# Optimization experiments

Hardware: AMD Instinct MI355X
Metric: run time of the kernel (lower is better)

## Reference

```python
import jax, jax.numpy as jnp
import numpy as np
import math

D_MODEL = 1024
NUM_HEADS = 16
D_K = D_MODEL // NUM_HEADS
SEQ_LEN = 2048
THETA = 10000.0


def _rope_tables(seq_len, d_k, theta):
    # inv_freq over even dims, angles repeated-interleaved to full d_k
    inv_freq = theta ** (-jnp.arange(0, d_k, 2, dtype=jnp.float32) / d_k)  # [d_k/2]
    pos = jnp.arange(seq_len, dtype=jnp.float32)                          # [s]
    angles = pos[:, None] * inv_freq[None, :]                             # [s, d_k/2]
    angles = jnp.repeat(angles, 2, axis=-1)                               # [s, d_k]
    return jnp.cos(angles), jnp.sin(angles)


def _rotate_half(x):
    # interleaved pairs: (x0,x1,x2,x3,...) -> (-x1,x0,-x3,x2,...)
    x_even = x[..., ::2]
    x_odd = x[..., 1::2]
    return jnp.stack([-x_odd, x_even], axis=-1).reshape(x.shape)


def _apply_rope(x, cos, sin):
    # x: [b, h, s, d_k]; cos/sin: [s, d_k]
    return x * cos + _rotate_half(x) * sin


def setup_inputs() -> dict:
    key = jax.random.key(0)
    ks = jax.random.split(key, 5)
    scale = 1.0 / math.sqrt(D_MODEL)
    X = jax.random.normal(ks[0], (2, SEQ_LEN, D_MODEL), dtype=jnp.float32)
    Wq = jax.random.normal(ks[1], (D_MODEL, D_MODEL), dtype=jnp.float32) * scale
    Wk = jax.random.normal(ks[2], (D_MODEL, D_MODEL), dtype=jnp.float32) * scale
    Wv = jax.random.normal(ks[3], (D_MODEL, D_MODEL), dtype=jnp.float32) * scale
    Wo = jax.random.normal(ks[4], (D_MODEL, D_MODEL), dtype=jnp.float32) * scale
    return {"X": X, "Wq": Wq, "Wk": Wk, "Wv": Wv, "Wo": Wo}


def reference(X, Wq, Wk, Wv, Wo):
    b, s, _ = X.shape
    h, dk = NUM_HEADS, D_K

    def proj(W):
        return (X @ W.T).reshape(b, s, h, dk).transpose(0, 2, 1, 3)  # [b,h,s,dk]

    q, k, v = proj(Wq), proj(Wk), proj(Wv)

    cos, sin = _rope_tables(s, dk, THETA)
    q = _apply_rope(q, cos, sin)
    k = _apply_rope(k, cos, sin)

    scores = jnp.einsum('bhid,bhjd->bhij', q, k) / math.sqrt(dk)
    causal = jnp.tril(jnp.ones((s, s), dtype=bool))
    scores = jnp.where(causal[None, None], scores, -jnp.inf)
    probs = jax.nn.softmax(scores, axis=-1)
    attended = jnp.einsum('bhij,bhjd->bhid', probs, v)               # [b,h,s,dk]

    out = attended.transpose(0, 2, 1, 3).reshape(b, s, h * dk)
    return out @ Wo.T
```

## Files before the change

kernel.cpp:

```cpp
#include <hip/hip_runtime.h>
#include <stdint.h>

#define D_MODEL 1024
#define NUM_HEADS 16
#define DK 64
#define SEQ 2048
#define BATCH 2
#define MROWS (BATCH * SEQ)
#define LOG2E 1.4426950408889634f
#define FIXM 14.0f

typedef short bf16x8 __attribute__((ext_vector_type(8)));
typedef float f32x4 __attribute__((ext_vector_type(4)));

__device__ __forceinline__ unsigned short f2bf(float f) {
    unsigned int u = __float_as_uint(f);
    u = (u + 0x7fffu + ((u >> 16) & 1u)) >> 16;
    return (unsigned short)u;
}
__device__ __forceinline__ unsigned short f2bf_trunc(float f) {
    return (unsigned short)(__float_as_uint(f) >> 16);
}
__device__ __forceinline__ float bf2f(unsigned short h) {
    return __uint_as_float(((unsigned int)h) << 16);
}
__device__ __forceinline__ void async16(const void* g, void* l) {
    __builtin_amdgcn_global_load_lds(
        (const __attribute__((address_space(1))) void*)g,
        (__attribute__((address_space(3))) void*)l, 16, 0, 0);
}
#define SWZ64(row, b) ((((row) * 8) + ((b) ^ ((row) & 7))) * 8)

__global__ void cast_all(const float4* __restrict__ X, const float4* __restrict__ Wq,
                         const float4* __restrict__ Wk, const float4* __restrict__ Wv,
                         const float4* __restrict__ Wo, ushort4* __restrict__ Xb,
                         ushort4* __restrict__ Wqkvb, ushort4* __restrict__ Wob) {
    int i = blockIdx.x * blockDim.x + threadIdx.x;
    const float4* src;
    ushort4* dst;
    int off;
    if (i < 1048576) { src = X; dst = Xb; off = i; }
    else if (i < 1310720) { src = Wq; dst = Wqkvb; off = i - 1048576; }
    else if (i < 1572864) { src = Wk; dst = Wqkvb + 262144; off = i - 1310720; }
    else if (i < 1835008) { src = Wv; dst = Wqkvb + 524288; off = i - 1572864; }
    else { src = Wo; dst = Wob; off = i - 1835008; }
    float4 v = src[off];
    ushort4 o;
    o.x = f2bf(v.x); o.y = f2bf(v.y); o.z = f2bf(v.z); o.w = f2bf(v.w);
    dst[off] = o;
}

__global__ __launch_bounds__(256) void gemm_qkv_rope(
    const unsigned short* __restrict__ A, const unsigned short* __restrict__ B,
    unsigned short* __restrict__ Qr, unsigned short* __restrict__ Kr,
    unsigned short* __restrict__ Vt) {
    __shared__ unsigned short As[128 * 64];
    __shared__ unsigned short Bs[128 * 64];
    const int K = D_MODEL, N = 3072;
    const int m0 = blockIdx.y * 128, n0 = blockIdx.x * 128;
    const int t = threadIdx.x;
    const int lane = t & 63, wave = t >> 6;
    const int mA = lane & 15, quad = lane >> 4;
    const int wr = (wave >> 1) * 64, wc = (wave & 1) * 64;

    f32x4 acc[4][4] = {};
    for (int k0 = 0; k0 < K; k0 += 64) {
#pragma unroll
        for (int i = 0; i < 4; ++i) {
            int ch = i * 256 + t;
            int r = ch >> 3, b = (ch & 7) ^ (r & 7);
            async16(A + (size_t)(m0 + r) * K + k0 + b * 8, (char*)As + ch * 16);
            async16(B + (size_t)(n0 + r) * K + k0 + b * 8, (char*)Bs + ch * 16);
        }
        __syncthreads();
#pragma unroll
        for (int kk = 0; kk < 2; ++kk) {
            bf16x8 af[4], bfr[4];
#pragma unroll
            for (int mi = 0; mi < 4; ++mi) {
                int rr = wr + mi * 16 + mA;
                af[mi] = *(const bf16x8*)&As[SWZ64(rr, kk * 4 + quad)];
            }
#pragma unroll
            for (int ni = 0; ni < 4; ++ni) {
                int rr = wc + ni * 16 + mA;
                bfr[ni] = *(const bf16x8*)&Bs[SWZ64(rr, kk * 4 + quad)];
            }
#pragma unroll
            for (int mi = 0; mi < 4; ++mi)
#pragma unroll
                for (int ni = 0; ni < 4; ++ni)
                    acc[mi][ni] = __builtin_amdgcn_mfma_f32_16x16x32_bf16(
                        af[mi], bfr[ni], acc[mi][ni], 0, 0, 0);
        }
        __syncthreads();
    }

    const int sec = n0 >> 10;
    if (sec == 2) {
#pragma unroll
        for (int mi = 0; mi < 4; ++mi)
#pragma unroll
            for (int ni = 0; ni < 4; ++ni) {
                int gm = m0 + wr + mi * 16 + quad * 4;
                int gn = n0 + wc + ni * 16 + mA;
                int d = gn & 1023, h = d >> 6, dk = d & 63;
                int b = gm >> 11, s = gm & 2047;
                ushort4 o;
                o.x = f2bf(acc[mi][ni][0]);
                o.y = f2bf(acc[mi][ni][1]);
                o.z = f2bf(acc[mi][ni][2]);
                o.w = f2bf(acc[mi][ni][3]);
                *(ushort4*)&Vt[((size_t)(b * NUM_HEADS + h) * DK + dk) * SEQ + s] = o;
            }
    } else {
        unsigned short* Dst = (sec == 0) ? Qr : Kr;
#pragma unroll
        for (int ni = 0; ni < 4; ++ni) {
            int gn = n0 + wc + ni * 16 + mA;
            int d = gn & 1023, h = d >> 6, dk = d & 63;
            float invf = __expf(-(float)(dk & ~1) * (9.210340371976184f / 64.0f));
            float sgn = (dk & 1) ? 1.0f : -1.0f;
#pragma unroll
            for (int mi = 0; mi < 4; ++mi) {
#pragma unroll
                for (int r = 0; r < 4; ++r) {
                    int gm = m0 + wr + mi * 16 + quad * 4 + r;
                    int b = gm >> 11, s = gm & 2047;
                    float sn, cs;
                    __sincosf((float)s * invf, &sn, &cs);
                    float val = acc[mi][ni][r];
                    float par = __shfl_xor(val, 1, 64);
                    float outv = val * cs + sgn * par * sn;
                    Dst[((size_t)(b * NUM_HEADS + h) * SEQ + s) * DK + dk] = f2bf(outv);
                }
            }
        }
    }
}

template <int TN, int OUT_BF16>
__global__ __launch_bounds__(256) void gemm_tile(
    const unsigned short* __restrict__ A, const unsigned short* __restrict__ B,
    void* __restrict__ Cout, int M, int N, int K) {
    __shared__ unsigned short As[128 * 64];
    __shared__ unsigned short Bs[TN * 64];
    const int m0 = blockIdx.y * 128, n0 = blockIdx.x * TN;
    const int t = threadIdx.x;
    const int lane = t & 63, wave = t >> 6;
    const int mA = lane & 15, quad = lane >> 4;
    constexpr int MI = (TN == 128) ? 4 : 2;
    constexpr int NI = 4;
    const int wr = (TN == 128) ? (wave >> 1) * 64 : wave * 32;
    const int wc = (TN == 128) ? (wave & 1) * 64 : 0;

    f32x4 acc[MI][NI] = {};
    for (int k0 = 0; k0 < K; k0 += 64) {
#pragma unroll
        for (int i = 0; i < 4; ++i) {
            int ch = i * 256 + t;
            int r = ch >> 3, b = (ch & 7) ^ (r & 7);
            async16(A + (size_t)(m0 + r) * K + k0 + b * 8, (char*)As + ch * 16);
        }
#pragma unroll
        for (int i = 0; i < TN / 32; ++i) {
            int ch = i * 256 + t;
            int r = ch >> 3, b = (ch & 7) ^ (r & 7);
            async16(B + (size_t)(n0 + r) * K + k0 + b * 8, (char*)Bs + ch * 16);
        }
        __syncthreads();
#pragma unroll
        for (int kk = 0; kk < 2; ++kk) {
            bf16x8 af[MI], bfr[NI];
#pragma unroll
            for (int mi = 0; mi < MI; ++mi) {
                int rr = wr + mi * 16 + mA;
                af[mi] = *(const bf16x8*)&As[SWZ64(rr, kk * 4 + quad)];
            }
#pragma unroll
            for (int ni = 0; ni < NI; ++ni) {
                int rr = wc + ni * 16 + mA;
                bfr[ni] = *(const bf16x8*)&Bs[SWZ64(rr, kk * 4 + quad)];
            }
#pragma unroll
            for (int mi = 0; mi < MI; ++mi)
#pragma unroll
                for (int ni = 0; ni < NI; ++ni)
                    acc[mi][ni] = __builtin_amdgcn_mfma_f32_16x16x32_bf16(
                        af[mi], bfr[ni], acc[mi][ni], 0, 0, 0);
        }
        __syncthreads();
    }
#pragma unroll
    for (int mi = 0; mi < MI; ++mi)
#pragma unroll
        for (int ni = 0; ni < NI; ++ni)
#pragma unroll
            for (int r = 0; r < 4; ++r) {
                int gm = m0 + wr + mi * 16 + quad * 4 + r;
                int gn = n0 + wc + ni * 16 + mA;
                if (OUT_BF16)
                    ((unsigned short*)Cout)[(size_t)gm * N + gn] = f2bf(acc[mi][ni][r]);
                else
                    ((float*)Cout)[(size_t)gm * N + gn] = acc[mi][ni][r];
            }
}

__global__ __launch_bounds__(256, 4) void flash_attn6(
    const unsigned short* __restrict__ Qr, const unsigned short* __restrict__ Kr,
    const unsigned short* __restrict__ Vt, unsigned short* __restrict__ Att) {
    __shared__ unsigned short Ks[2][64 * 64];
    __shared__ unsigned short Vs[2][64 * 64];
    __shared__ unsigned short Ps[4][16 * 64];
    const int bh = blockIdx.x;
    const int qt = 31 - (int)blockIdx.y;
    const int t = threadIdx.x;
    const int lane = t & 63, wave = t >> 6;
    const int mA = lane & 15, quad = lane >> 4;
    const int qr0 = qt * 64 + wave * 16;
    const size_t qkbase = (size_t)bh * SEQ * DK;
    const unsigned short* Kg = Kr + qkbase;
    const unsigned short* Vg = Vt + (size_t)bh * DK * SEQ;

    bf16x8 aq[2];
#pragma unroll
    for (int c = 0; c < 2; ++c) {
        bf16x8 raw = *(const bf16x8*)&Qr[qkbase + (size_t)(qr0 + mA) * DK + c * 32 + quad * 8];
        bf16x8 s;
#pragma unroll
        for (int j = 0; j < 8; ++j)
            s[j] = (short)f2bf(bf2f((unsigned short)raw[j]) * (0.125f * LOG2E));
        aq[c] = s;
    }

    f32x4 accT[4] = {};
    float lsum[4] = {};

#pragma unroll
    for (int i = 0; i < 2; ++i) {
        int ch = i * 256 + t;
        int row = ch >> 3, sb = (ch & 7) ^ (row & 7);
        async16(Kg + (size_t)row * DK + sb * 8, (char*)Ks[0] + ch * 16);
        async16(Vg + (size_t)row * SEQ + sb * 8, (char*)Vs[0] + ch * 16);
    }

    for (int jt = 0; jt <= qt; ++jt) {
        __syncthreads();
        const int cur = jt & 1;
        if (jt < qt) {
            const int j1 = (jt + 1) * 64;
#pragma unroll
            for (int i = 0; i < 2; ++i) {
                int ch = i * 256 + t;
                int row = ch >> 3, sb = (ch & 7) ^ (row & 7);
                async16(Kg + (size_t)(j1 + row) * DK + sb * 8, (char*)Ks[cur ^ 1] + ch * 16);
                async16(Vg + (size_t)row * SEQ + j1 + sb * 8, (char*)Vs[cur ^ 1] + ch * 16);
            }
        }
        const int j0 = jt * 64;
        const unsigned short* Kt = Ks[cur];
        const unsigned short* Vtile = Vs[cur];
        unsigned short* Pw = Ps[wave];

        f32x4 sc[4] = {};
#pragma unroll
        for (int js = 0; js < 4; ++js) {
            int row = js * 16 + mA;
            bf16x8 b0 = *(const bf16x8*)&Kt[SWZ64(row, quad)];
            bf16x8 b1 = *(const bf16x8*)&Kt[SWZ64(row, quad + 4)];
            sc[js] = __builtin_amdgcn_mfma_f32_16x16x32_bf16(aq[0], b0, sc[js], 0, 0, 0);
            sc[js] = __builtin_amdgcn_mfma_f32_16x16x32_bf16(aq[1], b1, sc[js], 0, 0, 0);
        }
        if (jt == qt) {
#pragma unroll
            for (int js = 0; js < 4; ++js) {
                int gcol = j0 + js * 16 + mA;
#pragma unroll
                for (int r = 0; r < 4; ++r)
                    if (gcol > qr0 + quad * 4 + r) sc[js][r] = -1e30f;
            }
        }

#pragma unroll
        for (int js = 0; js < 4; ++js)
#pragma unroll
            for (int r = 0; r < 4; ++r) {
                float p = __builtin_amdgcn_exp2f(sc[js][r] - FIXM);
                lsum[r] += p;
                int q = quad * 4 + r;
                Pw[SWZ64(q, js * 2 + (mA >> 3)) + (mA & 7)] = f2bf_trunc(p);
            }
        bf16x8 ap0 = *(const bf16x8*)&Pw[SWZ64(mA, quad)];
        bf16x8 ap1 = *(const bf16x8*)&Pw[SWZ64(mA, quad + 4)];
#pragma unroll
        for (int tn = 0; tn < 4; ++tn) {
            int row = tn * 16 + mA;
            bf16x8 bv0 = *(const bf16x8*)&Vtile[SWZ64(row, quad)];
            bf16x8 bv1 = *(const bf16x8*)&Vtile[SWZ64(row, quad + 4)];
            accT[tn] = __builtin_amdgcn_mfma_f32_16x16x32_bf16(bv0, ap0, accT[tn], 0, 0, 0);
            accT[tn] = __builtin_amdgcn_mfma_f32_16x16x32_bf16(bv1, ap1, accT[tn], 0, 0, 0);
        }
    }

#pragma unroll
    for (int r = 0; r < 4; ++r)
#pragma unroll
        for (int off = 1; off < 16; off <<= 1)
            lsum[r] += __shfl_xor(lsum[r], off, 64);
    __syncthreads();
    float* LL = (float*)Ks;
    if (mA == 0)
#pragma unroll
        for (int r = 0; r < 4; ++r) LL[wave * 16 + quad * 4 + r] = lsum[r];
    __syncthreads();
    const float rl = 1.0f / LL[wave * 16 + mA];

    const int b = bh >> 4, h = bh & 15;
#pragma unroll
    for (int tn = 0; tn < 4; ++tn) {
        ushort4 o;
        o.x = f2bf(accT[tn][0] * rl);
        o.y = f2bf(accT[tn][1] * rl);
        o.z = f2bf(accT[tn][2] * rl);
        o.w = f2bf(accT[tn][3] * rl);
        *(ushort4*)&Att[(size_t)(b * SEQ + qr0 + mA) * D_MODEL + h * DK + tn * 16 + quad * 4] = o;
    }
}

extern "C" void kernel_launch(void* const* d_in, const int* in_sizes, int n_in,
                              void* d_out, int out_size, void* d_ws, size_t ws_size,
                              hipStream_t stream) {
    const float* X = (const float*)d_in[0];
    const float* Wq = (const float*)d_in[1];
    const float* Wk = (const float*)d_in[2];
    const float* Wv = (const float*)d_in[3];
    const float* Wo = (const float*)d_in[4];

    char* ws = (char*)d_ws;
    unsigned short* Xb    = (unsigned short*)(ws + 0);
    unsigned short* Wqkvb = (unsigned short*)(ws + (8u << 20));
    unsigned short* Wob   = (unsigned short*)(ws + (14u << 20));
    unsigned short* Qr    = (unsigned short*)(ws + (16u << 20));
    unsigned short* Kr    = (unsigned short*)(ws + (24u << 20));
    unsigned short* Vt    = (unsigned short*)(ws + (32u << 20));
    unsigned short* Att   = (unsigned short*)(ws + (40u << 20));

    cast_all<<<8192, 256, 0, stream>>>((const float4*)X, (const float4*)Wq,
                                       (const float4*)Wk, (const float4*)Wv,
                                       (const float4*)Wo, (ushort4*)Xb,
                                       (ushort4*)Wqkvb, (ushort4*)Wob);

    gemm_qkv_rope<<<dim3(3072 / 128, MROWS / 128), 256, 0, stream>>>(
        Xb, Wqkvb, Qr, Kr, Vt);

    flash_attn6<<<dim3(BATCH * NUM_HEADS, 32), 256, 0, stream>>>(Qr, Kr, Vt, Att);

    gemm_tile<64, 0><<<dim3(D_MODEL / 64, MROWS / 128), 256, 0, stream>>>(
        Att, Wob, d_out, MROWS, D_MODEL, D_MODEL);
}
```

Measured before the change: 182.6 us.

## Enlarge flash-attention query tile and use precomputed RoPE table in QKV epilogue

```diff
diff --git a/kernel.cpp b/kernel.cpp
--- a/kernel.cpp
+++ b/kernel.cpp
@@ -34,34 +34,51 @@
 __global__ void cast_all(const float4* __restrict__ X, const float4* __restrict__ Wq,
                          const float4* __restrict__ Wk, const float4* __restrict__ Wv,
                          const float4* __restrict__ Wo, ushort4* __restrict__ Xb,
-                         ushort4* __restrict__ Wqkvb, ushort4* __restrict__ Wob) {
-    int i = blockIdx.x * blockDim.x + threadIdx.x;
-    const float4* src;
-    ushort4* dst;
-    int off;
-    if (i < 1048576) { src = X; dst = Xb; off = i; }
-    else if (i < 1310720) { src = Wq; dst = Wqkvb; off = i - 1048576; }
-    else if (i < 1572864) { src = Wk; dst = Wqkvb + 262144; off = i - 1310720; }
-    else if (i < 1835008) { src = Wv; dst = Wqkvb + 524288; off = i - 1572864; }
-    else { src = Wo; dst = Wob; off = i - 1835008; }
-    float4 v = src[off];
-    ushort4 o;
-    o.x = f2bf(v.x); o.y = f2bf(v.y); o.z = f2bf(v.z); o.w = f2bf(v.w);
-    dst[off] = o;
+                         ushort4* __restrict__ Wqkvb, ushort4* __restrict__ Wob,
+                         float2* __restrict__ RT) {
+    const int bx = blockIdx.x, t = threadIdx.x;
+    if (bx < 8192) {
+        int i = bx * 256 + t;
+        const float4* src;
+        ushort4* dst;
+        int off;
+        if (i < 1048576) { src = X; dst = Xb; off = i; }
+        else if (i < 1310720) { src = Wq; dst = Wqkvb; off = i - 1048576; }
+        else if (i < 1572864) { src = Wk; dst = Wqkvb + 262144; off = i - 1310720; }
+        else if (i < 1835008) { src = Wv; dst = Wqkvb + 524288; off = i - 1572864; }
+        else { src = Wo; dst = Wob; off = i - 1835008; }
+        float4 v = src[off];
+        ushort4 o;
+        o.x = f2bf(v.x); o.y = f2bf(v.y); o.z = f2bf(v.z); o.w = f2bf(v.w);
+        dst[off] = o;
+    } else {
+        int idx = (bx - 8192) * 256 + t;
+        int f = idx >> 9;
+        int s4 = (idx & 511) * 4;
+        float invf = __expf(-(float)(2 * f) * (9.210340371976184f / 64.0f));
+#pragma unroll
+        for (int j = 0; j < 4; ++j) {
+            int s = s4 + j;
+            float sn, cs;
+            __sincosf((float)s * invf, &sn, &cs);
+            RT[f * SEQ + s] = make_float2(cs, sn);
+        }
+    }
 }
 
 __global__ __launch_bounds__(256) void gemm_qkv_rope(
     const unsigned short* __restrict__ A, const unsigned short* __restrict__ B,
-    unsigned short* __restrict__ Qr, unsigned short* __restrict__ Kr,
-    unsigned short* __restrict__ Vt) {
+    const float2* __restrict__ RT, unsigned short* __restrict__ Qr,
+    unsigned short* __restrict__ Kr, unsigned short* __restrict__ Vt) {
     __shared__ unsigned short As[128 * 64];
     __shared__ unsigned short Bs[128 * 64];
-    const int K = D_MODEL, N = 3072;
+    const int K = D_MODEL;
     const int m0 = blockIdx.y * 128, n0 = blockIdx.x * 128;
     const int t = threadIdx.x;
     const int lane = t & 63, wave = t >> 6;
     const int mA = lane & 15, quad = lane >> 4;
     const int wr = (wave >> 1) * 64, wc = (wave & 1) * 64;
+    const int sec = n0 >> 10;
 
     f32x4 acc[4][4] = {};
     for (int k0 = 0; k0 < K; k0 += 64) {
@@ -86,17 +103,25 @@
                 int rr = wc + ni * 16 + mA;
                 bfr[ni] = *(const bf16x8*)&Bs[SWZ64(rr, kk * 4 + quad)];
             }
-#pragma unroll
-            for (int mi = 0; mi < 4; ++mi)
-#pragma unroll
-                for (int ni = 0; ni < 4; ++ni)
-                    acc[mi][ni] = __builtin_amdgcn_mfma_f32_16x16x32_bf16(
-                        af[mi], bfr[ni], acc[mi][ni], 0, 0, 0);
+            if (sec == 2) {
+#pragma unroll
+                for (int mi = 0; mi < 4; ++mi)
+#pragma unroll
+                    for (int ni = 0; ni < 4; ++ni)
+                        acc[mi][ni] = __builtin_amdgcn_mfma_f32_16x16x32_bf16(
+                            af[mi], bfr[ni], acc[mi][ni], 0, 0, 0);
+            } else {
+#pragma unroll
+                for (int mi = 0; mi < 4; ++mi)
+#pragma unroll
+                    for (int ni = 0; ni < 4; ++ni)
+                        acc[mi][ni] = __builtin_amdgcn_mfma_f32_16x16x32_bf16(
+                            bfr[ni], af[mi], acc[mi][ni], 0, 0, 0);
+            }
         }
         __syncthreads();
     }
 
-    const int sec = n0 >> 10;
     if (sec == 2) {
 #pragma unroll
         for (int mi = 0; mi < 4; ++mi)
@@ -116,24 +141,24 @@
     } else {
         unsigned short* Dst = (sec == 0) ? Qr : Kr;
 #pragma unroll
-        for (int ni = 0; ni < 4; ++ni) {
-            int gn = n0 + wc + ni * 16 + mA;
-            int d = gn & 1023, h = d >> 6, dk = d & 63;
-            float invf = __expf(-(float)(dk & ~1) * (9.210340371976184f / 64.0f));
-            float sgn = (dk & 1) ? 1.0f : -1.0f;
-#pragma unroll
-            for (int mi = 0; mi < 4; ++mi) {
-#pragma unroll
-                for (int r = 0; r < 4; ++r) {
-                    int gm = m0 + wr + mi * 16 + quad * 4 + r;
-                    int b = gm >> 11, s = gm & 2047;
-                    float sn, cs;
-                    __sincosf((float)s * invf, &sn, &cs);
-                    float val = acc[mi][ni][r];
-                    float par = __shfl_xor(val, 1, 64);
-                    float outv = val * cs + sgn * par * sn;
-                    Dst[((size_t)(b * NUM_HEADS + h) * SEQ + s) * DK + dk] = f2bf(outv);
-                }
+        for (int mi = 0; mi < 4; ++mi) {
+            int gm = m0 + wr + mi * 16 + mA;
+            int b = gm >> 11, s = gm & 2047;
+#pragma unroll
+            for (int ni = 0; ni < 4; ++ni) {
+                int gnb = n0 + wc + ni * 16 + quad * 4;
+                int h = (gnb >> 6) & 15, dkb = gnb & 63;
+                int f0 = dkb >> 1;
+                float2 t0 = RT[f0 * SEQ + s];
+                float2 t1 = RT[(f0 + 1) * SEQ + s];
+                float a0 = acc[mi][ni][0], a1 = acc[mi][ni][1];
+                float a2 = acc[mi][ni][2], a3 = acc[mi][ni][3];
+                ushort4 o;
+                o.x = f2bf(a0 * t0.x - a1 * t0.y);
+                o.y = f2bf(a1 * t0.x + a0 * t0.y);
+                o.z = f2bf(a2 * t1.x - a3 * t1.y);
+                o.w = f2bf(a3 * t1.x + a2 * t1.y);
+                *(ushort4*)&Dst[((size_t)(b * NUM_HEADS + h) * SEQ + s) * DK + dkb] = o;
             }
         }
     }
@@ -206,35 +231,41 @@
             }
 }
 
-__global__ __launch_bounds__(256, 4) void flash_attn6(
+__global__ __launch_bounds__(256, 2) void flash_attn8(
     const unsigned short* __restrict__ Qr, const unsigned short* __restrict__ Kr,
     const unsigned short* __restrict__ Vt, unsigned short* __restrict__ Att) {
     __shared__ unsigned short Ks[2][64 * 64];
     __shared__ unsigned short Vs[2][64 * 64];
-    __shared__ unsigned short Ps[4][16 * 64];
-    const int bh = blockIdx.x;
-    const int qt = 31 - (int)blockIdx.y;
+    __shared__ unsigned short Ps[4][32 * 64];
+    const int id = blockIdx.x;
+    const int bh = id & 31;
+    const int qt = 15 - (id >> 5);
     const int t = threadIdx.x;
     const int lane = t & 63, wave = t >> 6;
     const int mA = lane & 15, quad = lane >> 4;
-    const int qr0 = qt * 64 + wave * 16;
+    const int qr0 = qt * 128 + wave * 32;
+    const int myTile = 2 * qt + (wave >> 1);
+    const int jtLast = 2 * qt + 1;
     const size_t qkbase = (size_t)bh * SEQ * DK;
     const unsigned short* Kg = Kr + qkbase;
     const unsigned short* Vg = Vt + (size_t)bh * DK * SEQ;
 
-    bf16x8 aq[2];
-#pragma unroll
-    for (int c = 0; c < 2; ++c) {
-        bf16x8 raw = *(const bf16x8*)&Qr[qkbase + (size_t)(qr0 + mA) * DK + c * 32 + quad * 8];
-        bf16x8 s;
-#pragma unroll
-        for (int j = 0; j < 8; ++j)
-            s[j] = (short)f2bf(bf2f((unsigned short)raw[j]) * (0.125f * LOG2E));
-        aq[c] = s;
-    }
-
-    f32x4 accT[4] = {};
-    float lsum[4] = {};
+    bf16x8 aq[2][2];
+#pragma unroll
+    for (int rt = 0; rt < 2; ++rt)
+#pragma unroll
+        for (int c = 0; c < 2; ++c) {
+            bf16x8 raw = *(const bf16x8*)&Qr[qkbase + (size_t)(qr0 + rt * 16 + mA) * DK + c * 32 + quad * 8];
+            bf16x8 s;
+#pragma unroll
+            for (int j = 0; j < 8; ++j)
+                s[j] = (short)f2bf(bf2f((unsigned short)raw[j]) * (0.125f * LOG2E));
+            aq[rt][c] = s;
+        }
+
+    f32x4 accT[2][4] = {};
+    float lsum[2][4] = {};
+    unsigned short* Pw = Ps[wave];
 
 #pragma unroll
     for (int i = 0; i < 2; ++i) {
@@ -244,10 +275,10 @@
         async16(Vg + (size_t)row * SEQ + sb * 8, (char*)Vs[0] + ch * 16);
     }
 
-    for (int jt = 0; jt <= qt; ++jt) {
+    for (int jt = 0; jt <= jtLast; ++jt) {
         __syncthreads();
         const int cur = jt & 1;
-        if (jt < qt) {
+        if (jt < jtLast) {
             const int j1 = (jt + 1) * 64;
 #pragma unroll
             for (int i = 0; i < 2; ++i) {
@@ -257,73 +288,97 @@
                 async16(Vg + (size_t)row * SEQ + j1 + sb * 8, (char*)Vs[cur ^ 1] + ch * 16);
             }
         }
+        if (jt > myTile) continue;
+
         const int j0 = jt * 64;
         const unsigned short* Kt = Ks[cur];
         const unsigned short* Vtile = Vs[cur];
-        unsigned short* Pw = Ps[wave];
-
-        f32x4 sc[4] = {};
-#pragma unroll
-        for (int js = 0; js < 4; ++js) {
-            int row = js * 16 + mA;
-            bf16x8 b0 = *(const bf16x8*)&Kt[SWZ64(row, quad)];
-            bf16x8 b1 = *(const bf16x8*)&Kt[SWZ64(row, quad + 4)];
-            sc[js] = __builtin_amdgcn_mfma_f32_16x16x32_bf16(aq[0], b0, sc[js], 0, 0, 0);
-            sc[js] = __builtin_amdgcn_mfma_f32_16x16x32_bf16(aq[1], b1, sc[js], 0, 0, 0);
-        }
-        if (jt == qt) {
+
+        bf16x8 kf[4][2];
+#pragma unroll
+        for (int js = 0; js < 4; ++js)
+#pragma unroll
+            for (int c = 0; c < 2; ++c)
+                kf[js][c] = *(const bf16x8*)&Kt[SWZ64(js * 16 + mA, c * 4 + quad)];
+
+        f32x4 sc[2][4] = {};
+#pragma unroll
+        for (int rt = 0; rt < 2; ++rt)
 #pragma unroll
             for (int js = 0; js < 4; ++js) {
-                int gcol = j0 + js * 16 + mA;
-#pragma unroll
-                for (int r = 0; r < 4; ++r)
-                    if (gcol > qr0 + quad * 4 + r) sc[js][r] = -1e30f;
-            }
-        }
-
-#pragma unroll
-        for (int js = 0; js < 4; ++js)
-#pragma unroll
-            for (int r = 0; r < 4; ++r) {
-                float p = __builtin_amdgcn_exp2f(sc[js][r] - FIXM);
-                lsum[r] += p;
-                int q = quad * 4 + r;
-                Pw[SWZ64(q, js * 2 + (mA >> 3)) + (mA & 7)] = f2bf_trunc(p);
-            }
-        bf16x8 ap0 = *(const bf16x8*)&Pw[SWZ64(mA, quad)];
-        bf16x8 ap1 = *(const bf16x8*)&Pw[SWZ64(mA, quad + 4)];
+                sc[rt][js] = __builtin_amdgcn_mfma_f32_16x16x32_bf16(
+                    aq[rt][0], kf[js][0], sc[rt][js], 0, 0, 0);
+                sc[rt][js] = __builtin_amdgcn_mfma_f32_16x16x32_bf16(
+                    aq[rt][1], kf[js][1], sc[rt][js], 0, 0, 0);
+            }
+        if (jt == myTile) {
+#pragma unroll
+            for (int rt = 0; rt < 2; ++rt)
+#pragma unroll
+                for (int js = 0; js < 4; ++js) {
+                    int gcol = j0 + js * 16 + mA;
+#pragma unroll
+                    for (int r = 0; r < 4; ++r)
+                        if (gcol > qr0 + rt * 16 + quad * 4 + r) sc[rt][js][r] = -1e30f;
+                }
+        }
+
+#pragma unroll
+        for (int rt = 0; rt < 2; ++rt)
+#pragma unroll
+            for (int js = 0; js < 4; ++js)
+#pragma unroll
+                for (int r = 0; r < 4; ++r) {
+                    float p = __builtin_amdgcn_exp2f(sc[rt][js][r] - FIXM);
+                    lsum[rt][r] += p;
+                    int q = rt * 16 + quad * 4 + r;
+                    Pw[SWZ64(q, js * 2 + (mA >> 3)) + (mA & 7)] = f2bf_trunc(p);
+                }
+
+        bf16x8 vf[4][2];
+#pragma unroll
+        for (int tn = 0; tn < 4; ++tn)
+#pragma unroll
+            for (int c = 0; c < 2; ++c)
+                vf[tn][c] = *(const bf16x8*)&Vtile[SWZ64(tn * 16 + mA, c * 4 + quad)];
+#pragma unroll
+        for (int rt = 0; rt < 2; ++rt) {
+            bf16x8 ap0 = *(const bf16x8*)&Pw[SWZ64(rt * 16 + mA, quad)];
+            bf16x8 ap1 = *(const bf16x8*)&Pw[SWZ64(rt * 16 + mA, quad + 4)];
+#pragma unroll
+            for (int tn = 0; tn < 4; ++tn) {
+                accT[rt][tn] = __builtin_amdgcn_mfma_f32_16x16x32_bf16(
+                    vf[tn][0], ap0, accT[rt][tn], 0, 0, 0);
+                accT[rt][tn] = __builtin_amdgcn_mfma_f32_16x16x32_bf16(
+                    vf[tn][1], ap1, accT[rt][tn], 0, 0, 0);
+            }
+        }
+    }
+
+    const int b = bh >> 4, h = bh & 15;
+#pragma unroll
+    for (int rt = 0; rt < 2; ++rt) {
+#pragma unroll
+        for (int r = 0; r < 4; ++r)
+#pragma unroll
+            for (int off = 1; off < 16; off <<= 1)
+                lsum[rt][r] += __shfl_xor(lsum[rt][r], off, 64);
+        const int srcl = (mA >> 2) << 4;
+        float s0 = __shfl(lsum[rt][0], srcl), s1 = __shfl(lsum[rt][1], srcl);
+        float s2 = __shfl(lsum[rt][2], srcl), s3 = __shfl(lsum[rt][3], srcl);
+        const int rr = mA & 3;
+        float sum = (rr == 0) ? s0 : (rr == 1) ? s1 : (rr == 2) ? s2 : s3;
+        const float rl = 1.0f / sum;
+        const int q = qr0 + rt * 16 + mA;
 #pragma unroll
         for (int tn = 0; tn < 4; ++tn) {
-            int row = tn * 16 + mA;
-            bf16x8 bv0 = *(const bf16x8*)&Vtile[SWZ64(row, quad)];
-            bf16x8 bv1 = *(const bf16x8*)&Vtile[SWZ64(row, quad + 4)];
-            accT[tn] = __builtin_amdgcn_mfma_f32_16x16x32_bf16(bv0, ap0, accT[tn], 0, 0, 0);
-            accT[tn] = __builtin_amdgcn_mfma_f32_16x16x32_bf16(bv1, ap1, accT[tn], 0, 0, 0);
-        }
-    }
-
-#pragma unroll
-    for (int r = 0; r < 4; ++r)
-#pragma unroll
-        for (int off = 1; off < 16; off <<= 1)
-            lsum[r] += __shfl_xor(lsum[r], off, 64);
-    __syncthreads();
-    float* LL = (float*)Ks;
-    if (mA == 0)
-#pragma unroll
-        for (int r = 0; r < 4; ++r) LL[wave * 16 + quad * 4 + r] = lsum[r];
-    __syncthreads();
-    const float rl = 1.0f / LL[wave * 16 + mA];
-
-    const int b = bh >> 4, h = bh & 15;
-#pragma unroll
-    for (int tn = 0; tn < 4; ++tn) {
-        ushort4 o;
-        o.x = f2bf(accT[tn][0] * rl);
-        o.y = f2bf(accT[tn][1] * rl);
-        o.z = f2bf(accT[tn][2] * rl);
-        o.w = f2bf(accT[tn][3] * rl);
-        *(ushort4*)&Att[(size_t)(b * SEQ + qr0 + mA) * D_MODEL + h * DK + tn * 16 + quad * 4] = o;
+            ushort4 o;
+            o.x = f2bf(accT[rt][tn][0] * rl);
+            o.y = f2bf(accT[rt][tn][1] * rl);
+            o.z = f2bf(accT[rt][tn][2] * rl);
+            o.w = f2bf(accT[rt][tn][3] * rl);
+            *(ushort4*)&Att[(size_t)(b * SEQ + q) * D_MODEL + h * DK + tn * 16 + quad * 4] = o;
+        }
     }
 }
 
@@ -344,16 +399,17 @@
     unsigned short* Kr    = (unsigned short*)(ws + (24u << 20));
     unsigned short* Vt    = (unsigned short*)(ws + (32u << 20));
     unsigned short* Att   = (unsigned short*)(ws + (40u << 20));
-
-    cast_all<<<8192, 256, 0, stream>>>((const float4*)X, (const float4*)Wq,
-                                       (const float4*)Wk, (const float4*)Wv,
-                                       (const float4*)Wo, (ushort4*)Xb,
-                                       (ushort4*)Wqkvb, (ushort4*)Wob);
+    float2*         RT    = (float2*)(ws + (48u << 20));
+
+    cast_all<<<8192 + 64, 256, 0, stream>>>((const float4*)X, (const float4*)Wq,
+                                            (const float4*)Wk, (const float4*)Wv,
+                                            (const float4*)Wo, (ushort4*)Xb,
+                                            (ushort4*)Wqkvb, (ushort4*)Wob, RT);
 
     gemm_qkv_rope<<<dim3(3072 / 128, MROWS / 128), 256, 0, stream>>>(
-        Xb, Wqkvb, Qr, Kr, Vt);
-
-    flash_attn6<<<dim3(BATCH * NUM_HEADS, 32), 256, 0, stream>>>(Qr, Kr, Vt, Att);
+        Xb, Wqkvb, RT, Qr, Kr, Vt);
+
+    flash_attn8<<<512, 256, 0, stream>>>(Qr, Kr, Vt, Att);
 
     gemm_tile<64, 0><<<dim3(D_MODEL / 64, MROWS / 128), 256, 0, stream>>>(
         Att, Wob, d_out, MROWS, D_MODEL, D_MODEL);
```

After: 206.2 us. 12.9% more time.

## Precompute RoPE table and swap MFMA operands for vectorized Q/K stores

Applied to the files above, without the earlier changes.

```diff
diff --git a/kernel.cpp b/kernel.cpp
--- a/kernel.cpp
+++ b/kernel.cpp
@@ -34,30 +34,48 @@
 __global__ void cast_all(const float4* __restrict__ X, const float4* __restrict__ Wq,
                          const float4* __restrict__ Wk, const float4* __restrict__ Wv,
                          const float4* __restrict__ Wo, ushort4* __restrict__ Xb,
-                         ushort4* __restrict__ Wqkvb, ushort4* __restrict__ Wob) {
-    int i = blockIdx.x * blockDim.x + threadIdx.x;
-    const float4* src;
-    ushort4* dst;
-    int off;
-    if (i < 1048576) { src = X; dst = Xb; off = i; }
-    else if (i < 1310720) { src = Wq; dst = Wqkvb; off = i - 1048576; }
-    else if (i < 1572864) { src = Wk; dst = Wqkvb + 262144; off = i - 1310720; }
-    else if (i < 1835008) { src = Wv; dst = Wqkvb + 524288; off = i - 1572864; }
-    else { src = Wo; dst = Wob; off = i - 1835008; }
-    float4 v = src[off];
-    ushort4 o;
-    o.x = f2bf(v.x); o.y = f2bf(v.y); o.z = f2bf(v.z); o.w = f2bf(v.w);
-    dst[off] = o;
-}
-
-__global__ __launch_bounds__(256) void gemm_qkv_rope(
+                         ushort4* __restrict__ Wqkvb, ushort4* __restrict__ Wob,
+                         float2* __restrict__ RT) {
+    const int bx = blockIdx.x, t = threadIdx.x;
+    if (bx < 8192) {
+        int i = bx * 256 + t;
+        const float4* src;
+        ushort4* dst;
+        int off;
+        if (i < 1048576) { src = X; dst = Xb; off = i; }
+        else if (i < 1310720) { src = Wq; dst = Wqkvb; off = i - 1048576; }
+        else if (i < 1572864) { src = Wk; dst = Wqkvb + 262144; off = i - 1310720; }
+        else if (i < 1835008) { src = Wv; dst = Wqkvb + 524288; off = i - 1572864; }
+        else { src = Wo; dst = Wob; off = i - 1835008; }
+        float4 v = src[off];
+        ushort4 o;
+        o.x = f2bf(v.x); o.y = f2bf(v.y); o.z = f2bf(v.z); o.w = f2bf(v.w);
+        dst[off] = o;
+    } else {
+        int idx = (bx - 8192) * 256 + t;
+        int f = idx >> 9;
+        int s4 = (idx & 511) * 4;
+        float invf = __expf(-(float)(2 * f) * (9.210340371976184f / 64.0f));
+#pragma unroll
+        for (int j = 0; j < 4; ++j) {
+            int s = s4 + j;
+            float sn, cs;
+            __sincosf((float)s * invf, &sn, &cs);
+            RT[f * SEQ + s] = make_float2(cs, sn);
+        }
+    }
+}
+
+template <int SWAP>
+__global__ __launch_bounds__(256) void gemm_qkv(
     const unsigned short* __restrict__ A, const unsigned short* __restrict__ B,
-    unsigned short* __restrict__ Qr, unsigned short* __restrict__ Kr,
-    unsigned short* __restrict__ Vt) {
+    const float2* __restrict__ RT, unsigned short* __restrict__ Qr,
+    unsigned short* __restrict__ Kr, unsigned short* __restrict__ Vt,
+    int n_base) {
     __shared__ unsigned short As[128 * 64];
     __shared__ unsigned short Bs[128 * 64];
-    const int K = D_MODEL, N = 3072;
-    const int m0 = blockIdx.y * 128, n0 = blockIdx.x * 128;
+    const int K = D_MODEL;
+    const int m0 = blockIdx.y * 128, n0 = n_base + blockIdx.x * 128;
     const int t = threadIdx.x;
     const int lane = t & 63, wave = t >> 6;
     const int mA = lane & 15, quad = lane >> 4;
@@ -89,15 +107,19 @@
 #pragma unroll
             for (int mi = 0; mi < 4; ++mi)
 #pragma unroll
-                for (int ni = 0; ni < 4; ++ni)
-                    acc[mi][ni] = __builtin_amdgcn_mfma_f32_16x16x32_bf16(
-                        af[mi], bfr[ni], acc[mi][ni], 0, 0, 0);
-        }
-        __syncthreads();
-    }
-
-    const int sec = n0 >> 10;
-    if (sec == 2) {
+                for (int ni = 0; ni < 4; ++ni) {
+                    if (SWAP)
+                        acc[mi][ni] = __builtin_amdgcn_mfma_f32_16x16x32_bf16(
+                            bfr[ni], af[mi], acc[mi][ni], 0, 0, 0);
+                    else
+                        acc[mi][ni] = __builtin_amdgcn_mfma_f32_16x16x32_bf16(
+                            af[mi], bfr[ni], acc[mi][ni], 0, 0, 0);
+                }
+        }
+        __syncthreads();
+    }
+
+    if (!SWAP) {
 #pragma unroll
         for (int mi = 0; mi < 4; ++mi)
 #pragma unroll
@@ -114,26 +136,26 @@
                 *(ushort4*)&Vt[((size_t)(b * NUM_HEADS + h) * DK + dk) * SEQ + s] = o;
             }
     } else {
-        unsigned short* Dst = (sec == 0) ? Qr : Kr;
-#pragma unroll
-        for (int ni = 0; ni < 4; ++ni) {
-            int gn = n0 + wc + ni * 16 + mA;
-            int d = gn & 1023, h = d >> 6, dk = d & 63;
-            float invf = __expf(-(float)(dk & ~1) * (9.210340371976184f / 64.0f));
-            float sgn = (dk & 1) ? 1.0f : -1.0f;
-#pragma unroll
-            for (int mi = 0; mi < 4; ++mi) {
-#pragma unroll
-                for (int r = 0; r < 4; ++r) {
-                    int gm = m0 + wr + mi * 16 + quad * 4 + r;
-                    int b = gm >> 11, s = gm & 2047;
-                    float sn, cs;
-                    __sincosf((float)s * invf, &sn, &cs);
-                    float val = acc[mi][ni][r];
-                    float par = __shfl_xor(val, 1, 64);
-                    float outv = val * cs + sgn * par * sn;
-                    Dst[((size_t)(b * NUM_HEADS + h) * SEQ + s) * DK + dk] = f2bf(outv);
-                }
+        unsigned short* Dst = (n0 >> 10) == 0 ? Qr : Kr;
+#pragma unroll
+        for (int mi = 0; mi < 4; ++mi) {
+            int gm = m0 + wr + mi * 16 + mA;
+            int b = gm >> 11, s = gm & 2047;
+#pragma unroll
+            for (int ni = 0; ni < 4; ++ni) {
+                int gnb = n0 + wc + ni * 16 + quad * 4;
+                int h = (gnb >> 6) & 15, dkb = gnb & 63;
+                int f0 = dkb >> 1;
+                float2 t0 = RT[f0 * SEQ + s];
+                float2 t1 = RT[(f0 + 1) * SEQ + s];
+                float a0 = acc[mi][ni][0], a1 = acc[mi][ni][1];
+                float a2 = acc[mi][ni][2], a3 = acc[mi][ni][3];
+                ushort4 o;
+                o.x = f2bf(a0 * t0.x - a1 * t0.y);
+                o.y = f2bf(a1 * t0.x + a0 * t0.y);
+                o.z = f2bf(a2 * t1.x - a3 * t1.y);
+                o.w = f2bf(a3 * t1.x + a2 * t1.y);
+                *(ushort4*)&Dst[((size_t)(b * NUM_HEADS + h) * SEQ + s) * DK + dkb] = o;
             }
         }
     }
@@ -344,14 +366,17 @@
     unsigned short* Kr    = (unsigned short*)(ws + (24u << 20));
     unsigned short* Vt    = (unsigned short*)(ws + (32u << 20));
     unsigned short* Att   = (unsigned short*)(ws + (40u << 20));
-
-    cast_all<<<8192, 256, 0, stream>>>((const float4*)X, (const float4*)Wq,
-                                       (const float4*)Wk, (const float4*)Wv,
-                                       (const float4*)Wo, (ushort4*)Xb,
-                                       (ushort4*)Wqkvb, (ushort4*)Wob);
-
-    gemm_qkv_rope<<<dim3(3072 / 128, MROWS / 128), 256, 0, stream>>>(
-        Xb, Wqkvb, Qr, Kr, Vt);
+    float2*         RT    = (float2*)(ws + (48u << 20));
+
+    cast_all<<<8192 + 64, 256, 0, stream>>>((const float4*)X, (const float4*)Wq,
+                                            (const float4*)Wk, (const float4*)Wv,
+                                            (const float4*)Wo, (ushort4*)Xb,
+                                            (ushort4*)Wqkvb, (ushort4*)Wob, RT);
+
+    gemm_qkv<1><<<dim3(16, MROWS / 128), 256, 0, stream>>>(
+        Xb, Wqkvb, RT, Qr, Kr, Vt, 0);
+    gemm_qkv<0><<<dim3(8, MROWS / 128), 256, 0, stream>>>(
+        Xb, Wqkvb, RT, Qr, Kr, Vt, 2048);
 
     flash_attn6<<<dim3(BATCH * NUM_HEADS, 32), 256, 0, stream>>>(Qr, Kr, Vt, Att);
 
```

After: 188.4 us. 3.2% more time.
